# Kernel tuning notes

Measured on AMD Instinct MI355X. Metric: run time of the kernel, lower is better.

The kernel has to match this reference:

```python
import jax, jax.numpy as jnp
import numpy as np

B, Q, K, DQ, DK, DV, H = 16, 64, 512, 512, 512, 512, 256
MASK_VAL = -1e6


def setup_inputs() -> dict:
    key = jax.random.key(0)
    k1, k2, k3, k4, k5, k6, k7 = jax.random.split(key, 7)
    return {
        "queries": jax.random.normal(k1, (B, Q, DQ), dtype=jnp.float32),
        "keys": jax.random.normal(k2, (B, K, DK), dtype=jnp.float32),
        "values": jax.random.normal(k3, (B, K, DV), dtype=jnp.float32),
        "valid_lens": jax.random.randint(k4, (B,), 1, K + 1, dtype=jnp.int32),
        "Wq": jax.random.normal(k5, (DQ, H), dtype=jnp.float32) * (1.0 / np.sqrt(DQ)),
        "Wk": jax.random.normal(k6, (DK, H), dtype=jnp.float32) * (1.0 / np.sqrt(DK)),
        "Wv": jax.random.normal(k7, (H,), dtype=jnp.float32) * (1.0 / np.sqrt(H)),
    }


def reference(queries, keys, values, valid_lens, Wq, Wk, Wv):
    # Project queries and keys into the shared additive-attention space.
    q = jnp.einsum("bqd,dh->bqh", queries, Wq)   # [B,Q,H]
    k = jnp.einsum("bkd,dh->bkh", keys, Wk)      # [B,K,H]
    # Bahdanau additive scoring: tanh(q + k) projected to a scalar per (q,k).
    feats = jnp.tanh(q[:, :, None, :] + k[:, None, :, :])  # [B,Q,K,H]
    scores = jnp.einsum("bqkh,h->bqk", feats, Wv)           # [B,Q,K]
    # Masked softmax over the key axis (positions >= valid_len masked out).
    mask = jnp.arange(K)[None, None, :] < valid_lens[:, None, None]  # [B,1,K]
    scores = jnp.where(mask, scores, MASK_VAL)
    attn = jax.nn.softmax(scores, axis=-1)                  # [B,Q,K]
    # Dropout is identity in eval mode; weighted sum of values.
    return jnp.einsum("bqk,bkv->bqv", attn, values)         # [B,Q,DV]
```

## Files before the change

kernel.cpp:

```cpp
#include <hip/hip_runtime.h>

#define LOG2E 1.4426950408889634f
#define TWO_LOG2E 2.8853900817779268f

typedef __attribute__((ext_vector_type(8))) short short8;
typedef __attribute__((ext_vector_type(4))) float f32x4;

__device__ __forceinline__ float e2x(float v) {
    return __builtin_amdgcn_exp2f(v * TWO_LOG2E);
}

__device__ __forceinline__ void split2(float x, float y, unsigned& hi, unsigned& lo) {
    unsigned ux = __float_as_uint(x), uy = __float_as_uint(y);
    float hx = __uint_as_float(ux & 0xffff0000u);
    float hy = __uint_as_float(uy & 0xffff0000u);
    unsigned lx = __float_as_uint(x - hx), ly = __float_as_uint(y - hy);
    hi = (ux >> 16) | (uy & 0xffff0000u);
    lo = (lx >> 16) | (ly & 0xffff0000u);
}

__global__ __launch_bounds__(256) void wprep_kernel(const float* __restrict__ Wq,
                                                    const float* __restrict__ Wk,
                                                    ushort* __restrict__ Wq2T,
                                                    ushort* __restrict__ Wk2T) {
    __shared__ float T[64][65];
    const float* W  = blockIdx.z ? Wk : Wq;
    ushort* W2T     = blockIdx.z ? Wk2T : Wq2T;
    const int t  = threadIdx.x;
    const int k0 = blockIdx.x * 64;
    const int n0 = blockIdx.y * 64;
#pragma unroll
    for (int p = 0; p < 4; ++p) {
        int u  = t + p * 256;
        int kk = u >> 4;
        int nf = (u & 15) * 4;
        float4 w = *reinterpret_cast<const float4*>(&W[(size_t)(k0 + kk) * 256 + n0 + nf]);
        T[nf + 0][kk] = w.x; T[nf + 1][kk] = w.y;
        T[nf + 2][kk] = w.z; T[nf + 3][kk] = w.w;
    }
    __syncthreads();
#pragma unroll
    for (int p = 0; p < 4; ++p) {
        int u  = t + p * 256;
        int n  = u >> 4;
        int kf = (u & 15) * 4;
        float a = T[n][kf], b = T[n][kf + 1], c = T[n][kf + 2], d = T[n][kf + 3];
        unsigned h01, l01, h23, l23;
        split2(a, b, h01, l01);
        split2(c, d, h23, l23);
        int kg = k0 + kf;
        ushort* row = W2T + (size_t)(n0 + n) * 1536 + (kg >> 5) * 96 + (kg & 31);
        uint2 hi; hi.x = h01; hi.y = h23;
        uint2 lo; lo.x = l01; lo.y = l23;
        *reinterpret_cast<uint2*>(row)      = hi;
        *reinterpret_cast<uint2*>(row + 32) = hi;
        *reinterpret_cast<uint2*>(row + 64) = lo;
    }
}

__global__ __launch_bounds__(256) void mfma_proj_kernel(const float* __restrict__ queries,
                                                        const float* __restrict__ keys,
                                                        const ushort* __restrict__ Wq2T,
                                                        const ushort* __restrict__ Wk2T,
                                                        float* __restrict__ Eq,
                                                        float* __restrict__ Ekp) {
    __shared__ float smemf[9216];
    ushort* Ah = reinterpret_cast<ushort*>(smemf);
    ushort* Ws = reinterpret_cast<ushort*>(smemf) + 12288;

    const int t    = threadIdx.x;
    const int mt   = blockIdx.x;
    const int Nb   = blockIdx.y * 64;
    const bool isQ = mt < 8;
    const int Mb   = mt * 128;
    const float4* Asrc4 = reinterpret_cast<const float4*>(isQ ? queries : keys)
                        + (size_t)(isQ ? Mb : Mb - 1024) * 128;
    const ushort* W2T = isQ ? Wq2T : Wk2T;

    const int ln15 = t & 15;
    const int q    = (t >> 4) & 3;
    const int w    = t >> 6;
    const int wm   = (w >> 1) * 64;
    const int wn   = (w & 1) * 32;

    int bn[3], brem[3];
#pragma unroll
    for (int i = 0; i < 3; ++i) {
        int o   = i * 4096 + (t >> 6) * 1024 + (t & 63) * 16;
        bn[i]   = o / 192;
        brem[i] = o - bn[i] * 192;
    }
    const char* gB[3];
#pragma unroll
    for (int i = 0; i < 3; ++i)
        gB[i] = reinterpret_cast<const char*>(W2T) + (size_t)(Nb + bn[i]) * 3072 + brem[i];

    f32x4 acc[4][2];
#pragma unroll
    for (int fm = 0; fm < 4; ++fm)
#pragma unroll
        for (int fn = 0; fn < 2; ++fn) acc[fm][fn] = (f32x4)0.0f;

    for (int c = 0; c < 16; ++c) {
        __syncthreads();
#pragma unroll
        for (int p = 0; p < 4; ++p) {
            int u  = t + p * 256;
            int m  = u >> 3;
            int kf = (u & 7) * 4;
            float4 a = Asrc4[(size_t)m * 128 + c * 8 + (u & 7)];
            unsigned h01, l01, h23, l23;
            split2(a.x, a.y, h01, l01);
            split2(a.z, a.w, h23, l23);
            uint2 hi; hi.x = h01; hi.y = h23;
            uint2 lo; lo.x = l01; lo.y = l23;
            ushort* row = Ah + m * 96 + kf;
            *reinterpret_cast<uint2*>(row)      = hi;
            *reinterpret_cast<uint2*>(row + 32) = lo;
            *reinterpret_cast<uint2*>(row + 64) = hi;
        }
#pragma unroll
        for (int i = 0; i < 3; ++i) {
            __builtin_amdgcn_global_load_lds(
                reinterpret_cast<const unsigned int*>(gB[i]),
                reinterpret_cast<unsigned int*>(
                    reinterpret_cast<char*>(Ws) + i * 4096 + (t >> 6) * 1024),
                16, 0, 0);
            gB[i] += 192;
        }
        __syncthreads();
#pragma unroll
        for (int s = 0; s < 3; ++s) {
            short8 af[4], bf[2];
#pragma unroll
            for (int fm = 0; fm < 4; ++fm)
                af[fm] = *reinterpret_cast<const short8*>(
                    Ah + (wm + fm * 16 + ln15) * 96 + s * 32 + q * 8);
#pragma unroll
            for (int fn = 0; fn < 2; ++fn)
                bf[fn] = *reinterpret_cast<const short8*>(
                    Ws + (wn + fn * 16 + ln15) * 96 + s * 32 + q * 8);
#pragma unroll
            for (int fm = 0; fm < 4; ++fm)
#pragma unroll
                for (int fn = 0; fn < 2; ++fn)
                    acc[fm][fn] = __builtin_amdgcn_mfma_f32_16x16x32_bf16(
                        af[fm], bf[fn], acc[fm][fn], 0, 0, 0);
        }
    }

    if (isQ) {
#pragma unroll
        for (int fm = 0; fm < 4; ++fm)
#pragma unroll
            for (int fn = 0; fn < 2; ++fn)
#pragma unroll
                for (int r = 0; r < 4; ++r) {
                    int row = Mb + wm + fm * 16 + q * 4 + r;
                    int col = Nb + wn + fn * 16 + ln15;
                    Eq[(size_t)row * 256 + col] = e2x(acc[fm][fn][r]);
                }
    } else {
        __syncthreads();
        float (*Cs)[131] = reinterpret_cast<float(*)[131]>(smemf);
#pragma unroll
        for (int fm = 0; fm < 4; ++fm)
#pragma unroll
            for (int fn = 0; fn < 2; ++fn)
#pragma unroll
                for (int r = 0; r < 4; ++r) {
                    int m_l = wm + fm * 16 + q * 4 + r;
                    int n_l = wn + fn * 16 + ln15;
                    Cs[n_l][m_l] = acc[fm][fn][r];
                }
        __syncthreads();
        const int rk     = Mb - 1024;
        const int b      = rk >> 9;
        const int k0h    = (rk & 511) >> 1;
        const int h2base = Nb >> 1;
        float4* out4 = reinterpret_cast<float4*>(Ekp);
#pragma unroll
        for (int p = 0; p < 8; ++p) {
            int u   = t + p * 256;
            int h2r = u >> 6;
            int kp  = u & 63;
            int kk  = kp * 2;
            float4 o;
            o.x = e2x(Cs[2 * h2r    ][kk    ]);
            o.y = e2x(Cs[2 * h2r + 1][kk    ]);
            o.z = e2x(Cs[2 * h2r    ][kk + 1]);
            o.w = e2x(Cs[2 * h2r + 1][kk + 1]);
            out4[(size_t)b * 32768 + (size_t)(h2base + h2r) * 256 + k0h + kp] = o;
        }
    }
}

__global__ __launch_bounds__(256) void score_softmax_kernel(
        const float* __restrict__ Eq, const float* __restrict__ Ekp,
        const float* __restrict__ Wv, const int* __restrict__ valid_lens,
        float* __restrict__ attn) {
    __shared__ float redmA[4], redmB[4], redlA[4], redlB[4];

    const int t  = threadIdx.x;
    const int bq = blockIdx.x;
    const int b  = bq >> 5;
    const int q0 = (bq & 31) * 2;

    const float* eqA = Eq + (size_t)(b * 64 + q0) * 256;
    const float* eqB = eqA + 256;
    const float4* ek4 = reinterpret_cast<const float4*>(Ekp) + (size_t)b * 32768 + t;

    float accA0 = 0.f, accA1 = 0.f, accB0 = 0.f, accB1 = 0.f;
#pragma unroll 4
    for (int h2 = 0; h2 < 128; ++h2) {
        const float4 ek = ek4[h2 * 256];
        const float w0 = Wv[2 * h2];
        const float w1 = Wv[2 * h2 + 1];
        {
            const float e0 = eqA[2 * h2], e1 = eqA[2 * h2 + 1];
            float a00 = fmaf(e0, ek.x, 1.0f);
            float a10 = fmaf(e1, ek.y, 1.0f);
            float a01 = fmaf(e0, ek.z, 1.0f);
            float a11 = fmaf(e1, ek.w, 1.0f);
            float d0 = a00 * a10, d1 = a01 * a11;
            float n0 = fmaf(w1, a00, w0 * a10);
            float n1 = fmaf(w1, a01, w0 * a11);
            accA0 = fmaf(n0, __builtin_amdgcn_rcpf(d0), accA0);
            accA1 = fmaf(n1, __builtin_amdgcn_rcpf(d1), accA1);
        }
        {
            const float e0 = eqB[2 * h2], e1 = eqB[2 * h2 + 1];
            float a00 = fmaf(e0, ek.x, 1.0f);
            float a10 = fmaf(e1, ek.y, 1.0f);
            float a01 = fmaf(e0, ek.z, 1.0f);
            float a11 = fmaf(e1, ek.w, 1.0f);
            float d0 = a00 * a10, d1 = a01 * a11;
            float n0 = fmaf(w1, a00, w0 * a10);
            float n1 = fmaf(w1, a01, w0 * a11);
            accB0 = fmaf(n0, __builtin_amdgcn_rcpf(d0), accB0);
            accB1 = fmaf(n1, __builtin_amdgcn_rcpf(d1), accB1);
        }
    }
    float sA0 = -2.0f * accA0, sA1 = -2.0f * accA1;
    float sB0 = -2.0f * accB0, sB1 = -2.0f * accB1;
    const int vl = valid_lens[b];
    const int k0 = 2 * t;
    if (k0     >= vl) { sA0 = -1e6f; sB0 = -1e6f; }
    if (k0 + 1 >= vl) { sA1 = -1e6f; sB1 = -1e6f; }

    const int w = t >> 6;
    float mA = fmaxf(sA0, sA1);
    float mB = fmaxf(sB0, sB1);
#pragma unroll
    for (int off = 32; off > 0; off >>= 1) {
        mA = fmaxf(mA, __shfl_xor(mA, off));
        mB = fmaxf(mB, __shfl_xor(mB, off));
    }
    if ((t & 63) == 0) { redmA[w] = mA; redmB[w] = mB; }
    __syncthreads();
    mA = fmaxf(fmaxf(redmA[0], redmA[1]), fmaxf(redmA[2], redmA[3]));
    mB = fmaxf(fmaxf(redmB[0], redmB[1]), fmaxf(redmB[2], redmB[3]));

    float pA0 = __builtin_amdgcn_exp2f((sA0 - mA) * LOG2E);
    float pA1 = __builtin_amdgcn_exp2f((sA1 - mA) * LOG2E);
    float pB0 = __builtin_amdgcn_exp2f((sB0 - mB) * LOG2E);
    float pB1 = __builtin_amdgcn_exp2f((sB1 - mB) * LOG2E);
    float lA = pA0 + pA1, lB = pB0 + pB1;
#pragma unroll
    for (int off = 32; off > 0; off >>= 1) {
        lA += __shfl_xor(lA, off);
        lB += __shfl_xor(lB, off);
    }
    if ((t & 63) == 0) { redlA[w] = lA; redlB[w] = lB; }
    __syncthreads();
    lA = (redlA[0] + redlA[1]) + (redlA[2] + redlA[3]);
    lB = (redlB[0] + redlB[1]) + (redlB[2] + redlB[3]);
    const float invA = 1.0f / lA;
    const float invB = 1.0f / lB;

    float2* attn2 = reinterpret_cast<float2*>(attn);
    float2 oA; oA.x = pA0 * invA; oA.y = pA1 * invA;
    float2 oB; oB.x = pB0 * invB; oB.y = pB1 * invB;
    attn2[(size_t)(b * 64 + q0) * 256 + t]       = oA;
    attn2[(size_t)(b * 64 + q0 + 1) * 256 + t]   = oB;
}

__global__ __launch_bounds__(256) void pv_kernel(const float* __restrict__ attn,
                                                 const float* __restrict__ values,
                                                 float* __restrict__ out) {
    __shared__ float attnS[4][512];
    const int t   = threadIdx.x;
    const int b   = blockIdx.z;
    const int q0  = blockIdx.y * 4;
    const int v4b = blockIdx.x * 32;

    const float4* attn4 = reinterpret_cast<const float4*>(attn) + (size_t)(b * 64 + q0) * 128;
#pragma unroll
    for (int p = 0; p < 2; ++p) {
        int u  = t + p * 256;
        int qr = u >> 7;
        int c4 = u & 127;
        *reinterpret_cast<float4*>(&attnS[qr][c4 * 4]) = attn4[qr * 128 + c4];
    }
    __syncthreads();

    const int kh = t >> 7;
    const int q  = (t >> 5) & 3;
    const int v4 = v4b + (t & 31);
    const float* arow = &attnS[q][kh * 256];
    const float4* vp = reinterpret_cast<const float4*>(values)
                     + ((size_t)b * 512 + (size_t)kh * 256) * 128 + v4;

    float ax = 0.f, ay = 0.f, az = 0.f, aw = 0.f;
    float4 n0 = vp[0], n1 = vp[128], n2 = vp[256], n3 = vp[384];
#pragma unroll 2
    for (int kk = 0; kk < 256; kk += 4) {
        float4 c0 = n0, c1 = n1, c2 = n2, c3 = n3;
        vp += 512;
        if (kk + 4 < 256) { n0 = vp[0]; n1 = vp[128]; n2 = vp[256]; n3 = vp[384]; }
        float4 a = *reinterpret_cast<const float4*>(&arow[kk]);
        ax = fmaf(a.x, c0.x, ax); ay = fmaf(a.x, c0.y, ay);
        az = fmaf(a.x, c0.z, az); aw = fmaf(a.x, c0.w, aw);
        ax = fmaf(a.y, c1.x, ax); ay = fmaf(a.y, c1.y, ay);
        az = fmaf(a.y, c1.z, az); aw = fmaf(a.y, c1.w, aw);
        ax = fmaf(a.z, c2.x, ax); ay = fmaf(a.z, c2.y, ay);
        az = fmaf(a.z, c2.z, az); aw = fmaf(a.z, c2.w, aw);
        ax = fmaf(a.w, c3.x, ax); ay = fmaf(a.w, c3.y, ay);
        az = fmaf(a.w, c3.z, az); aw = fmaf(a.w, c3.w, aw);
    }

    __syncthreads();
    float* red = &attnS[0][0];
    if (kh == 1) {
        float4 o; o.x = ax; o.y = ay; o.z = az; o.w = aw;
        *reinterpret_cast<float4*>(&red[(t - 128) * 4]) = o;
    }
    __syncthreads();
    if (kh == 0) {
        float4 o = *reinterpret_cast<const float4*>(&red[t * 4]);
        o.x += ax; o.y += ay; o.z += az; o.w += aw;
        reinterpret_cast<float4*>(out)[(size_t)(b * 64 + q0 + q) * 128 + v4] = o;
    }
}

extern "C" void kernel_launch(void* const* d_in, const int* in_sizes, int n_in,
                              void* d_out, int out_size, void* d_ws, size_t ws_size,
                              hipStream_t stream) {
    (void)in_sizes; (void)n_in; (void)out_size; (void)ws_size;
    const float* queries    = (const float*)d_in[0];
    const float* keys       = (const float*)d_in[1];
    const float* values     = (const float*)d_in[2];
    const int*   valid_lens = (const int*)d_in[3];
    const float* Wq         = (const float*)d_in[4];
    const float* Wk         = (const float*)d_in[5];
    const float* Wv         = (const float*)d_in[6];
    float* out = (float*)d_out;

    float* ws    = (float*)d_ws;
    float* Eq    = ws;
    float* Ekp   = ws + 262144;
    float* attn  = ws + 262144 + 2097152;
    ushort* Wq2T = (ushort*)(ws + 2883584);
    ushort* Wk2T = Wq2T + 393216;

    hipLaunchKernelGGL(wprep_kernel, dim3(8, 4, 2), dim3(256), 0, stream,
                       Wq, Wk, Wq2T, Wk2T);
    hipLaunchKernelGGL(mfma_proj_kernel, dim3(72, 4), dim3(256), 0, stream,
                       queries, keys, Wq2T, Wk2T, Eq, Ekp);
    hipLaunchKernelGGL(score_softmax_kernel, dim3(512), dim3(256), 0, stream,
                       Eq, Ekp, Wv, valid_lens, attn);
    hipLaunchKernelGGL(pv_kernel, dim3(4, 16, 16), dim3(256), 0, stream, attn, values, out);
}
```

Measured before the change: 166.2 us.

## Tile PV matmul through shared memory with register-prefetched attn and value chunks

Rewrites the attention-times-values kernel as a shared-memory tiled GEMM. Each block now handles 32 queries by 64 value columns and streams 64-key chunks of attn and values through LDS. The next chunk is prefetched into registers while the current one is computed, and partial sums over key subgroups are reduced with wave shuffles. This cuts the repeated global reads of values, which the old layout re-fetched for every group of 4 queries, at the cost of fewer blocks (256 instead of 1024) and more registers per thread.

Result: faster. 153.8 us (-7.5%).

```diff
diff --git a/kernel.cpp b/kernel.cpp
--- a/kernel.cpp
+++ b/kernel.cpp
@@ -288,58 +288,112 @@
 __global__ __launch_bounds__(256) void pv_kernel(const float* __restrict__ attn,
                                                  const float* __restrict__ values,
                                                  float* __restrict__ out) {
-    __shared__ float attnS[4][512];
-    const int t   = threadIdx.x;
-    const int b   = blockIdx.z;
-    const int q0  = blockIdx.y * 4;
-    const int v4b = blockIdx.x * 32;
+    __shared__ __align__(16) float Ps[32][68];
+    __shared__ __align__(16) float Vs[64][68];
+
+    const int t  = threadIdx.x;
+    const int b  = blockIdx.z;
+    const int q0 = blockIdx.y * 32;
+    const int vt = blockIdx.x;
 
     const float4* attn4 = reinterpret_cast<const float4*>(attn) + (size_t)(b * 64 + q0) * 128;
-#pragma unroll
-    for (int p = 0; p < 2; ++p) {
-        int u  = t + p * 256;
-        int qr = u >> 7;
-        int c4 = u & 127;
-        *reinterpret_cast<float4*>(&attnS[qr][c4 * 4]) = attn4[qr * 128 + c4];
-    }
-    __syncthreads();
-
-    const int kh = t >> 7;
-    const int q  = (t >> 5) & 3;
-    const int v4 = v4b + (t & 31);
-    const float* arow = &attnS[q][kh * 256];
-    const float4* vp = reinterpret_cast<const float4*>(values)
-                     + ((size_t)b * 512 + (size_t)kh * 256) * 128 + v4;
-
-    float ax = 0.f, ay = 0.f, az = 0.f, aw = 0.f;
-    float4 n0 = vp[0], n1 = vp[128], n2 = vp[256], n3 = vp[384];
-#pragma unroll 2
-    for (int kk = 0; kk < 256; kk += 4) {
-        float4 c0 = n0, c1 = n1, c2 = n2, c3 = n3;
-        vp += 512;
-        if (kk + 4 < 256) { n0 = vp[0]; n1 = vp[128]; n2 = vp[256]; n3 = vp[384]; }
-        float4 a = *reinterpret_cast<const float4*>(&arow[kk]);
-        ax = fmaf(a.x, c0.x, ax); ay = fmaf(a.x, c0.y, ay);
-        az = fmaf(a.x, c0.z, az); aw = fmaf(a.x, c0.w, aw);
-        ax = fmaf(a.y, c1.x, ax); ay = fmaf(a.y, c1.y, ay);
-        az = fmaf(a.y, c1.z, az); aw = fmaf(a.y, c1.w, aw);
-        ax = fmaf(a.z, c2.x, ax); ay = fmaf(a.z, c2.y, ay);
-        az = fmaf(a.z, c2.z, az); aw = fmaf(a.z, c2.w, aw);
-        ax = fmaf(a.w, c3.x, ax); ay = fmaf(a.w, c3.y, ay);
-        az = fmaf(a.w, c3.z, az); aw = fmaf(a.w, c3.w, aw);
-    }
-
-    __syncthreads();
-    float* red = &attnS[0][0];
-    if (kh == 1) {
-        float4 o; o.x = ax; o.y = ay; o.z = az; o.w = aw;
-        *reinterpret_cast<float4*>(&red[(t - 128) * 4]) = o;
-    }
-    __syncthreads();
-    if (kh == 0) {
-        float4 o = *reinterpret_cast<const float4*>(&red[t * 4]);
-        o.x += ax; o.y += ay; o.z += az; o.w += aw;
-        reinterpret_cast<float4*>(out)[(size_t)(b * 64 + q0 + q) * 128 + v4] = o;
+    const float4* val4  = reinterpret_cast<const float4*>(values) + (size_t)b * 512 * 128 + vt * 16;
+
+    const int lane = t & 63;
+    const int w    = t >> 6;
+    const int v4   = lane & 15;
+    const int ksub = lane >> 4;
+
+    const int pq = t >> 4;
+    float4 rp[2], rv[4];
+
+#pragma unroll
+    for (int i = 0; i < 2; ++i) {
+        int u = t + i * 256;
+        rp[i] = attn4[(size_t)(u >> 4) * 128 + (u & 15)];
+    }
+#pragma unroll
+    for (int i = 0; i < 4; ++i) {
+        int u = t + i * 256;
+        rv[i] = val4[(size_t)(u >> 4) * 128 + (u & 15)];
+    }
+
+    float4 acc[8];
+#pragma unroll
+    for (int j = 0; j < 8; ++j) acc[j] = make_float4(0.f, 0.f, 0.f, 0.f);
+
+    for (int c = 0; c < 8; ++c) {
+        __syncthreads();
+#pragma unroll
+        for (int i = 0; i < 2; ++i) {
+            int u = t + i * 256;
+            *reinterpret_cast<float4*>(&Ps[u >> 4][(u & 15) * 4]) = rp[i];
+        }
+#pragma unroll
+        for (int i = 0; i < 4; ++i) {
+            int u = t + i * 256;
+            *reinterpret_cast<float4*>(&Vs[u >> 4][(u & 15) * 4]) = rv[i];
+        }
+        __syncthreads();
+        if (c < 7) {
+            int kf4 = (c + 1) * 16;
+#pragma unroll
+            for (int i = 0; i < 2; ++i) {
+                int u = t + i * 256;
+                rp[i] = attn4[(size_t)(u >> 4) * 128 + kf4 + (u & 15)];
+            }
+#pragma unroll
+            for (int i = 0; i < 4; ++i) {
+                int u = t + i * 256;
+                rv[i] = val4[(size_t)((c + 1) * 64 + (u >> 4)) * 128 + (u & 15)];
+            }
+        }
+#pragma unroll
+        for (int kk = 0; kk < 4; ++kk) {
+            int kb = kk * 16 + ksub * 4;
+            float4 V0 = *reinterpret_cast<const float4*>(&Vs[kb + 0][v4 * 4]);
+            float4 V1 = *reinterpret_cast<const float4*>(&Vs[kb + 1][v4 * 4]);
+            float4 V2 = *reinterpret_cast<const float4*>(&Vs[kb + 2][v4 * 4]);
+            float4 V3 = *reinterpret_cast<const float4*>(&Vs[kb + 3][v4 * 4]);
+#pragma unroll
+            for (int j = 0; j < 8; ++j) {
+                float4 p4 = *reinterpret_cast<const float4*>(&Ps[w * 8 + j][kb]);
+                acc[j].x = fmaf(p4.x, V0.x, acc[j].x);
+                acc[j].y = fmaf(p4.x, V0.y, acc[j].y);
+                acc[j].z = fmaf(p4.x, V0.z, acc[j].z);
+                acc[j].w = fmaf(p4.x, V0.w, acc[j].w);
+                acc[j].x = fmaf(p4.y, V1.x, acc[j].x);
+                acc[j].y = fmaf(p4.y, V1.y, acc[j].y);
+                acc[j].z = fmaf(p4.y, V1.z, acc[j].z);
+                acc[j].w = fmaf(p4.y, V1.w, acc[j].w);
+                acc[j].x = fmaf(p4.z, V2.x, acc[j].x);
+                acc[j].y = fmaf(p4.z, V2.y, acc[j].y);
+                acc[j].z = fmaf(p4.z, V2.z, acc[j].z);
+                acc[j].w = fmaf(p4.z, V2.w, acc[j].w);
+                acc[j].x = fmaf(p4.w, V3.x, acc[j].x);
+                acc[j].y = fmaf(p4.w, V3.y, acc[j].y);
+                acc[j].z = fmaf(p4.w, V3.z, acc[j].z);
+                acc[j].w = fmaf(p4.w, V3.w, acc[j].w);
+            }
+        }
+    }
+
+#pragma unroll
+    for (int j = 0; j < 8; ++j) {
+        acc[j].x += __shfl_xor(acc[j].x, 16);
+        acc[j].y += __shfl_xor(acc[j].y, 16);
+        acc[j].z += __shfl_xor(acc[j].z, 16);
+        acc[j].w += __shfl_xor(acc[j].w, 16);
+        acc[j].x += __shfl_xor(acc[j].x, 32);
+        acc[j].y += __shfl_xor(acc[j].y, 32);
+        acc[j].z += __shfl_xor(acc[j].z, 32);
+        acc[j].w += __shfl_xor(acc[j].w, 32);
+    }
+    if (ksub == 0) {
+        float4* out4 = reinterpret_cast<float4*>(out);
+#pragma unroll
+        for (int j = 0; j < 8; ++j)
+            out4[(size_t)(b * 64 + q0 + w * 8 + j) * 128 + vt * 16 + v4] = acc[j];
     }
 }
 
@@ -369,5 +423,5 @@
                        queries, keys, Wq2T, Wk2T, Eq, Ekp);
     hipLaunchKernelGGL(score_softmax_kernel, dim3(512), dim3(256), 0, stream,
                        Eq, Ekp, Wv, valid_lens, attn);
-    hipLaunchKernelGGL(pv_kernel, dim3(4, 16, 16), dim3(256), 0, stream, attn, values, out);
-}
+    hipLaunchKernelGGL(pv_kernel, dim3(8, 2, 16), dim3(256), 0, stream, attn, values, out);
+}
```

## Retile projection GEMM to 32x128 blocks and restage PV through shared memory

Applied to the files above, without the earlier changes.

The projection kernel moves from 128x64 tiles on a 72x4 grid to 32x128 tiles on a 288x2 grid. This gives more, smaller blocks with less LDS each, to improve occupancy and spread work across CUs. The PV kernel is rewritten to stage 64-key chunks of values and 8 query rows of attention in shared memory, with register prefetch of the next chunk. Each value tile is now reused across 8 queries rather than 4, which halves redundant value reads from global memory, in exchange for more syncs and LDS traffic. The smaller projection tiles re-read weight tiles more often.

Result: slower. 182.0 us (+9.5%).

```diff
diff --git a/kernel.cpp b/kernel.cpp
--- a/kernel.cpp
+++ b/kernel.cpp
@@ -64,51 +64,45 @@
                                                         const ushort* __restrict__ Wk2T,
                                                         float* __restrict__ Eq,
                                                         float* __restrict__ Ekp) {
-    __shared__ float smemf[9216];
+    __shared__ float smemf[7680];
     ushort* Ah = reinterpret_cast<ushort*>(smemf);
-    ushort* Ws = reinterpret_cast<ushort*>(smemf) + 12288;
+    ushort* Ws = reinterpret_cast<ushort*>(smemf) + 3072;
 
     const int t    = threadIdx.x;
     const int mt   = blockIdx.x;
-    const int Nb   = blockIdx.y * 64;
-    const bool isQ = mt < 8;
-    const int Mb   = mt * 128;
+    const int Nb   = blockIdx.y * 128;
+    const bool isQ = mt < 32;
+    const int mloc = (isQ ? mt : mt - 32) * 32;
     const float4* Asrc4 = reinterpret_cast<const float4*>(isQ ? queries : keys)
-                        + (size_t)(isQ ? Mb : Mb - 1024) * 128;
+                        + (size_t)mloc * 128;
     const ushort* W2T = isQ ? Wq2T : Wk2T;
 
     const int ln15 = t & 15;
     const int q    = (t >> 4) & 3;
     const int w    = t >> 6;
-    const int wm   = (w >> 1) * 64;
-    const int wn   = (w & 1) * 32;
-
-    int bn[3], brem[3];
-#pragma unroll
-    for (int i = 0; i < 3; ++i) {
-        int o   = i * 4096 + (t >> 6) * 1024 + (t & 63) * 16;
-        bn[i]   = o / 192;
-        brem[i] = o - bn[i] * 192;
-    }
-    const char* gB[3];
-#pragma unroll
-    for (int i = 0; i < 3; ++i)
-        gB[i] = reinterpret_cast<const char*>(W2T) + (size_t)(Nb + bn[i]) * 3072 + brem[i];
-
-    f32x4 acc[4][2];
-#pragma unroll
-    for (int fm = 0; fm < 4; ++fm)
+    const int wn   = w * 32;
+
+    const char* gB[6];
+#pragma unroll
+    for (int i = 0; i < 6; ++i) {
+        int o   = i * 4096 + t * 16;
+        int row = o / 192;
+        int rem = o - row * 192;
+        gB[i] = reinterpret_cast<const char*>(W2T) + (size_t)(Nb + row) * 3072 + rem;
+    }
+
+    f32x4 acc[2][2];
+#pragma unroll
+    for (int fm = 0; fm < 2; ++fm)
 #pragma unroll
         for (int fn = 0; fn < 2; ++fn) acc[fm][fn] = (f32x4)0.0f;
 
     for (int c = 0; c < 16; ++c) {
         __syncthreads();
-#pragma unroll
-        for (int p = 0; p < 4; ++p) {
-            int u  = t + p * 256;
-            int m  = u >> 3;
-            int kf = (u & 7) * 4;
-            float4 a = Asrc4[(size_t)m * 128 + c * 8 + (u & 7)];
+        {
+            int m  = t >> 3;
+            int kf = (t & 7) * 4;
+            float4 a = Asrc4[(size_t)m * 128 + c * 8 + (t & 7)];
             unsigned h01, l01, h23, l23;
             split2(a.x, a.y, h01, l01);
             split2(a.z, a.w, h23, l23);
@@ -120,28 +114,28 @@
             *reinterpret_cast<uint2*>(row + 64) = hi;
         }
 #pragma unroll
-        for (int i = 0; i < 3; ++i) {
+        for (int i = 0; i < 6; ++i) {
             __builtin_amdgcn_global_load_lds(
                 reinterpret_cast<const unsigned int*>(gB[i]),
                 reinterpret_cast<unsigned int*>(
-                    reinterpret_cast<char*>(Ws) + i * 4096 + (t >> 6) * 1024),
+                    reinterpret_cast<char*>(Ah) + 6144 + i * 4096 + (t >> 6) * 1024),
                 16, 0, 0);
             gB[i] += 192;
         }
         __syncthreads();
 #pragma unroll
         for (int s = 0; s < 3; ++s) {
-            short8 af[4], bf[2];
-#pragma unroll
-            for (int fm = 0; fm < 4; ++fm)
+            short8 af[2], bf[2];
+#pragma unroll
+            for (int fm = 0; fm < 2; ++fm)
                 af[fm] = *reinterpret_cast<const short8*>(
-                    Ah + (wm + fm * 16 + ln15) * 96 + s * 32 + q * 8);
+                    Ah + (fm * 16 + ln15) * 96 + s * 32 + q * 8);
 #pragma unroll
             for (int fn = 0; fn < 2; ++fn)
                 bf[fn] = *reinterpret_cast<const short8*>(
                     Ws + (wn + fn * 16 + ln15) * 96 + s * 32 + q * 8);
 #pragma unroll
-            for (int fm = 0; fm < 4; ++fm)
+            for (int fm = 0; fm < 2; ++fm)
 #pragma unroll
                 for (int fn = 0; fn < 2; ++fn)
                     acc[fm][fn] = __builtin_amdgcn_mfma_f32_16x16x32_bf16(
@@ -151,39 +145,38 @@
 
     if (isQ) {
 #pragma unroll
-        for (int fm = 0; fm < 4; ++fm)
+        for (int fm = 0; fm < 2; ++fm)
 #pragma unroll
             for (int fn = 0; fn < 2; ++fn)
 #pragma unroll
                 for (int r = 0; r < 4; ++r) {
-                    int row = Mb + wm + fm * 16 + q * 4 + r;
+                    int row = mloc + fm * 16 + q * 4 + r;
                     int col = Nb + wn + fn * 16 + ln15;
                     Eq[(size_t)row * 256 + col] = e2x(acc[fm][fn][r]);
                 }
     } else {
         __syncthreads();
-        float (*Cs)[131] = reinterpret_cast<float(*)[131]>(smemf);
-#pragma unroll
-        for (int fm = 0; fm < 4; ++fm)
+        float (*Cs)[33] = reinterpret_cast<float(*)[33]>(smemf);
+#pragma unroll
+        for (int fm = 0; fm < 2; ++fm)
 #pragma unroll
             for (int fn = 0; fn < 2; ++fn)
 #pragma unroll
                 for (int r = 0; r < 4; ++r) {
-                    int m_l = wm + fm * 16 + q * 4 + r;
+                    int m_l = fm * 16 + q * 4 + r;
                     int n_l = wn + fn * 16 + ln15;
                     Cs[n_l][m_l] = acc[fm][fn][r];
                 }
         __syncthreads();
-        const int rk     = Mb - 1024;
-        const int b      = rk >> 9;
-        const int k0h    = (rk & 511) >> 1;
+        const int b      = mloc >> 9;
+        const int k0h    = (mloc & 511) >> 1;
         const int h2base = Nb >> 1;
         float4* out4 = reinterpret_cast<float4*>(Ekp);
 #pragma unroll
-        for (int p = 0; p < 8; ++p) {
+        for (int p = 0; p < 4; ++p) {
             int u   = t + p * 256;
-            int h2r = u >> 6;
-            int kp  = u & 63;
+            int h2r = u >> 4;
+            int kp  = u & 15;
             int kk  = kp * 2;
             float4 o;
             o.x = e2x(Cs[2 * h2r    ][kk    ]);
@@ -288,58 +281,88 @@
 __global__ __launch_bounds__(256) void pv_kernel(const float* __restrict__ attn,
                                                  const float* __restrict__ values,
                                                  float* __restrict__ out) {
-    __shared__ float attnS[4][512];
-    const int t   = threadIdx.x;
-    const int b   = blockIdx.z;
-    const int q0  = blockIdx.y * 4;
-    const int v4b = blockIdx.x * 32;
+    __shared__ __align__(16) float Ps[8][68];
+    __shared__ __align__(16) float Vs[64][132];
+
+    const int t  = threadIdx.x;
+    const int b  = blockIdx.z;
+    const int q0 = blockIdx.y * 8;
+    const int vt = blockIdx.x;
 
     const float4* attn4 = reinterpret_cast<const float4*>(attn) + (size_t)(b * 64 + q0) * 128;
-#pragma unroll
-    for (int p = 0; p < 2; ++p) {
-        int u  = t + p * 256;
-        int qr = u >> 7;
-        int c4 = u & 127;
-        *reinterpret_cast<float4*>(&attnS[qr][c4 * 4]) = attn4[qr * 128 + c4];
-    }
-    __syncthreads();
-
-    const int kh = t >> 7;
-    const int q  = (t >> 5) & 3;
-    const int v4 = v4b + (t & 31);
-    const float* arow = &attnS[q][kh * 256];
-    const float4* vp = reinterpret_cast<const float4*>(values)
-                     + ((size_t)b * 512 + (size_t)kh * 256) * 128 + v4;
-
-    float ax = 0.f, ay = 0.f, az = 0.f, aw = 0.f;
-    float4 n0 = vp[0], n1 = vp[128], n2 = vp[256], n3 = vp[384];
-#pragma unroll 2
-    for (int kk = 0; kk < 256; kk += 4) {
-        float4 c0 = n0, c1 = n1, c2 = n2, c3 = n3;
-        vp += 512;
-        if (kk + 4 < 256) { n0 = vp[0]; n1 = vp[128]; n2 = vp[256]; n3 = vp[384]; }
-        float4 a = *reinterpret_cast<const float4*>(&arow[kk]);
-        ax = fmaf(a.x, c0.x, ax); ay = fmaf(a.x, c0.y, ay);
-        az = fmaf(a.x, c0.z, az); aw = fmaf(a.x, c0.w, aw);
-        ax = fmaf(a.y, c1.x, ax); ay = fmaf(a.y, c1.y, ay);
-        az = fmaf(a.y, c1.z, az); aw = fmaf(a.y, c1.w, aw);
-        ax = fmaf(a.z, c2.x, ax); ay = fmaf(a.z, c2.y, ay);
-        az = fmaf(a.z, c2.z, az); aw = fmaf(a.z, c2.w, aw);
-        ax = fmaf(a.w, c3.x, ax); ay = fmaf(a.w, c3.y, ay);
-        az = fmaf(a.w, c3.z, az); aw = fmaf(a.w, c3.w, aw);
-    }
-
-    __syncthreads();
-    float* red = &attnS[0][0];
-    if (kh == 1) {
-        float4 o; o.x = ax; o.y = ay; o.z = az; o.w = aw;
-        *reinterpret_cast<float4*>(&red[(t - 128) * 4]) = o;
-    }
-    __syncthreads();
-    if (kh == 0) {
-        float4 o = *reinterpret_cast<const float4*>(&red[t * 4]);
-        o.x += ax; o.y += ay; o.z += az; o.w += aw;
-        reinterpret_cast<float4*>(out)[(size_t)(b * 64 + q0 + q) * 128 + v4] = o;
+    const float4* val4  = reinterpret_cast<const float4*>(values) + (size_t)b * 512 * 128 + vt * 32;
+
+    const int lane = t & 63;
+    const int w    = t >> 6;
+    const int v4   = lane & 31;
+    const int ksub = lane >> 5;
+
+    float4 rp, rv[8];
+    if (t < 128) rp = attn4[(size_t)(t >> 4) * 128 + (t & 15)];
+#pragma unroll
+    for (int i = 0; i < 8; ++i) {
+        int u = t + i * 256;
+        rv[i] = val4[(size_t)(u >> 5) * 128 + (u & 31)];
+    }
+
+    float4 acc0 = make_float4(0.f, 0.f, 0.f, 0.f);
+    float4 acc1 = make_float4(0.f, 0.f, 0.f, 0.f);
+
+    for (int c = 0; c < 8; ++c) {
+        __syncthreads();
+        if (t < 128)
+            *reinterpret_cast<float4*>(&Ps[t >> 4][(t & 15) * 4]) = rp;
+#pragma unroll
+        for (int i = 0; i < 8; ++i) {
+            int u = t + i * 256;
+            *reinterpret_cast<float4*>(&Vs[u >> 5][(u & 31) * 4]) = rv[i];
+        }
+        __syncthreads();
+        if (c < 7) {
+            if (t < 128)
+                rp = attn4[(size_t)(t >> 4) * 128 + (c + 1) * 16 + (t & 15)];
+#pragma unroll
+            for (int i = 0; i < 8; ++i) {
+                int u = t + i * 256;
+                rv[i] = val4[(size_t)((c + 1) * 64 + (u >> 5)) * 128 + (u & 31)];
+            }
+        }
+#pragma unroll
+        for (int kk = 0; kk < 8; ++kk) {
+            int kb = kk * 8 + ksub * 4;
+            float4 V0 = *reinterpret_cast<const float4*>(&Vs[kb + 0][v4 * 4]);
+            float4 V1 = *reinterpret_cast<const float4*>(&Vs[kb + 1][v4 * 4]);
+            float4 V2 = *reinterpret_cast<const float4*>(&Vs[kb + 2][v4 * 4]);
+            float4 V3 = *reinterpret_cast<const float4*>(&Vs[kb + 3][v4 * 4]);
+            float4 p0 = *reinterpret_cast<const float4*>(&Ps[2 * w][kb]);
+            float4 p1 = *reinterpret_cast<const float4*>(&Ps[2 * w + 1][kb]);
+            acc0.x = fmaf(p0.x, V0.x, acc0.x); acc0.y = fmaf(p0.x, V0.y, acc0.y);
+            acc0.z = fmaf(p0.x, V0.z, acc0.z); acc0.w = fmaf(p0.x, V0.w, acc0.w);
+            acc0.x = fmaf(p0.y, V1.x, acc0.x); acc0.y = fmaf(p0.y, V1.y, acc0.y);
+            acc0.z = fmaf(p0.y, V1.z, acc0.z); acc0.w = fmaf(p0.y, V1.w, acc0.w);
+            acc0.x = fmaf(p0.z, V2.x, acc0.x); acc0.y = fmaf(p0.z, V2.y, acc0.y);
+            acc0.z = fmaf(p0.z, V2.z, acc0.z); acc0.w = fmaf(p0.z, V2.w, acc0.w);
+            acc0.x = fmaf(p0.w, V3.x, acc0.x); acc0.y = fmaf(p0.w, V3.y, acc0.y);
+            acc0.z = fmaf(p0.w, V3.z, acc0.z); acc0.w = fmaf(p0.w, V3.w, acc0.w);
+            acc1.x = fmaf(p1.x, V0.x, acc1.x); acc1.y = fmaf(p1.x, V0.y, acc1.y);
+            acc1.z = fmaf(p1.x, V0.z, acc1.z); acc1.w = fmaf(p1.x, V0.w, acc1.w);
+            acc1.x = fmaf(p1.y, V1.x, acc1.x); acc1.y = fmaf(p1.y, V1.y, acc1.y);
+            acc1.z = fmaf(p1.y, V1.z, acc1.z); acc1.w = fmaf(p1.y, V1.w, acc1.w);
+            acc1.x = fmaf(p1.z, V2.x, acc1.x); acc1.y = fmaf(p1.z, V2.y, acc1.y);
+            acc1.z = fmaf(p1.z, V2.z, acc1.z); acc1.w = fmaf(p1.z, V2.w, acc1.w);
+            acc1.x = fmaf(p1.w, V3.x, acc1.x); acc1.y = fmaf(p1.w, V3.y, acc1.y);
+            acc1.z = fmaf(p1.w, V3.z, acc1.z); acc1.w = fmaf(p1.w, V3.w, acc1.w);
+        }
+    }
+
+    acc0.x += __shfl_xor(acc0.x, 32); acc0.y += __shfl_xor(acc0.y, 32);
+    acc0.z += __shfl_xor(acc0.z, 32); acc0.w += __shfl_xor(acc0.w, 32);
+    acc1.x += __shfl_xor(acc1.x, 32); acc1.y += __shfl_xor(acc1.y, 32);
+    acc1.z += __shfl_xor(acc1.z, 32); acc1.w += __shfl_xor(acc1.w, 32);
+    if (ksub == 0) {
+        float4* out4 = reinterpret_cast<float4*>(out);
+        out4[(size_t)(b * 64 + q0 + 2 * w) * 128 + vt * 32 + v4]     = acc0;
+        out4[(size_t)(b * 64 + q0 + 2 * w + 1) * 128 + vt * 32 + v4] = acc1;
     }
 }
 
@@ -365,9 +388,9 @@
 
     hipLaunchKernelGGL(wprep_kernel, dim3(8, 4, 2), dim3(256), 0, stream,
                        Wq, Wk, Wq2T, Wk2T);
-    hipLaunchKernelGGL(mfma_proj_kernel, dim3(72, 4), dim3(256), 0, stream,
+    hipLaunchKernelGGL(mfma_proj_kernel, dim3(288, 2), dim3(256), 0, stream,
                        queries, keys, Wq2T, Wk2T, Eq, Ekp);
     hipLaunchKernelGGL(score_softmax_kernel, dim3(512), dim3(256), 0, stream,
                        Eq, Ekp, Wv, valid_lens, attn);
-    hipLaunchKernelGGL(pv_kernel, dim3(4, 16, 16), dim3(256), 0, stream, attn, values, out);
-}
+    hipLaunchKernelGGL(pv_kernel, dim3(4, 8, 16), dim3(256), 0, stream, attn, values, out);
+}
```
